# Kernel optimization log

Measured on AMD Instinct MI355X. Metric: run time of the kernel, lower is better.

## Reference

```python
import jax, jax.numpy as jnp
import numpy as np

B, S, D = 2, 2048, 2048
H = 16
I = 8192  # intermediate_size
HD = I // H  # per-head intermediate dim = 512


def setup_inputs() -> dict:
    key = jax.random.key(0)
    ks = jax.random.split(key, 7)
    scale_d = 1.0 / np.sqrt(D)
    scale_i = 1.0 / np.sqrt(I)
    return {
        "x": jax.random.normal(ks[0], (B, S, D), dtype=jnp.float32),
        "adjacency": jax.random.uniform(ks[1], (B, H, S, S), dtype=jnp.float32) * (1.0 / S),
        "Wg": jax.random.normal(ks[2], (D, I), dtype=jnp.float32) * scale_d,
        "Wu": jax.random.normal(ks[3], (D, I), dtype=jnp.float32) * scale_d,
        "Wd": jax.random.normal(ks[4], (I, D), dtype=jnp.float32) * scale_i,
        "eps": jnp.zeros((H,), dtype=jnp.float32),
        "alpha": jnp.ones((H,), dtype=jnp.float32),
    }


def reference(x, adjacency, Wg, Wu, Wd, eps, alpha):
    # gate/up projections + SwiGLU: (B,S,I)
    gate = jnp.einsum("bsd,di->bsi", x, Wg)
    up = jnp.einsum("bsd,di->bsi", x, Wu)
    h_inter = jax.nn.silu(gate) * up
    # split into heads: (B,H,S,HD)
    h_heads = h_inter.reshape(B, S, H, HD).transpose(0, 2, 1, 3)
    # batched per-head GIN: (1+eps_h)*h + alpha_h * A_h @ h, all heads at once
    agg = jnp.einsum("bhst,bhtd->bhsd", adjacency, h_heads)
    e = (1.0 + eps)[None, :, None, None]
    a = alpha[None, :, None, None]
    h_gin = e * h_heads + a * agg
    # recombine heads -> (B,S,I), then down projection
    h_comb = h_gin.transpose(0, 2, 1, 3).reshape(B, S, I)
    return jnp.einsum("bsi,id->bsd", h_comb, Wd)
```

## Files before the change

### kernel.cpp

```cpp
#include <hip/hip_runtime.h>
#include <hip/hip_bf16.h>


typedef __bf16 bf16x8 __attribute__((ext_vector_type(8)));
typedef float f32x4 __attribute__((ext_vector_type(4)));

__device__ __forceinline__ unsigned short f2bf(float f) {
    union { float f; unsigned int u; } x; x.f = f;
    unsigned int r = x.u + 0x7fffu + ((x.u >> 16) & 1u);
    return (unsigned short)(r >> 16);
}
__device__ __forceinline__ float bf2f(unsigned short b) {
    union { unsigned int u; float f; } x; x.u = ((unsigned int)b) << 16;
    return x.f;
}

__device__ __forceinline__ void gload_lds16(const void* g, void* l) {
    __builtin_amdgcn_global_load_lds((const __attribute__((address_space(1))) void*)g,
                                     (__attribute__((address_space(3))) void*)l,
                                     16, 0, 0);
}


__global__ void conv_kernel(const float* __restrict__ in, unsigned short* __restrict__ out) {
    size_t i = ((size_t)blockIdx.x * 256 + threadIdx.x) * 4;
    float4 v = *(const float4*)(in + i);
    ushort4 o; o.x = f2bf(v.x); o.y = f2bf(v.y); o.z = f2bf(v.z); o.w = f2bf(v.w);
    *(ushort4*)(out + i) = o;
}

__global__ void tconv_kernel(const float* __restrict__ in, unsigned short* __restrict__ out,
                             int R, int C) {
    __shared__ float tile[64][65];
    int nbc = C >> 6;
    int bc = blockIdx.x % nbc, br = blockIdx.x / nbc;
    int r0 = br * 64, c0 = bc * 64;
    int t = threadIdx.x;
#pragma unroll
    for (int i = 0; i < 4; ++i) {
        int idx = i * 256 + t;
        int r = idx >> 4, c4 = (idx & 15) * 4;
        float4 v = *(const float4*)(in + (size_t)(r0 + r) * C + c0 + c4);
        tile[r][c4] = v.x; tile[r][c4 + 1] = v.y; tile[r][c4 + 2] = v.z; tile[r][c4 + 3] = v.w;
    }
    __syncthreads();
#pragma unroll
    for (int i = 0; i < 4; ++i) {
        int idx = i * 256 + t;
        int c = idx >> 4, r4 = (idx & 15) * 4;
        ushort4 o;
        o.x = f2bf(tile[r4][c]); o.y = f2bf(tile[r4 + 1][c]);
        o.z = f2bf(tile[r4 + 2][c]); o.w = f2bf(tile[r4 + 3][c]);
        *(ushort4*)(out + (size_t)(c0 + c) * R + r0 + r4) = o;
    }
}

__global__ void __launch_bounds__(512, 2) gemm_gu(
    const unsigned short* __restrict__ xb,
    const unsigned short* __restrict__ WgT,
    const unsigned short* __restrict__ WuT,
    unsigned short* __restrict__ hhT)
{
    const int K = 2048;
    __shared__ unsigned short LDS[4][16384];
    int bid = (int)blockIdx.x;
    int lb = (bid & 7) * 128 + (bid >> 3);
    int mt = lb >> 6, nt = lb & 63;
    int tid = threadIdx.x, lane = tid & 63, wave = tid >> 6;
    int wm = wave >> 1, wn = wave & 1;
    int l15 = lane & 15, l4 = lane >> 4;

    f32x4 accg[4][4] = {};
    f32x4 accu[4][4] = {};

    int jl = (lane & 7) ^ (lane >> 3);
    int prowA = wave * 16 + (lane >> 3);
    int rowA0 = prowA + ((jl & 4) << 5);
    int ccA = (jl & 3) << 3;
    const unsigned short* srcA0 = xb + (size_t)(mt * 256 + rowA0) * K + ccA;
    const unsigned short* srcA1 = srcA0 + (size_t)8 * K;
    int prowB = tid >> 3;
    int jbl = (tid & 7) ^ (prowB & 7);
    int rowB0 = prowB + ((jbl & 4) << 4);
    int ccB = (jbl & 3) << 3;
    const unsigned short* srcBg = WgT + (size_t)(nt * 128 + rowB0) * K + ccB;
    const unsigned short* srcBu = WuT + (size_t)(nt * 128 + rowB0) * K + ccB;

    int cA0 = ((wm & 1) * 64 + l15) * 128 + (((((wm >> 1) << 2) + l4) ^ (l15 & 7)) << 4);
    int cB0 = l15 * 128 + ((((wn << 2) + l4) ^ (l15 & 7)) << 4);

#define GU_STAGE_A(t_) do {                                                              \
        char* dA = (char*)&LDS[(t_) & 3][0] + wave * 2048;                               \
        gload_lds16((const void*)(srcA0 + (size_t)(t_) * 32), (void*)dA);                \
        gload_lds16((const void*)(srcA1 + (size_t)(t_) * 32), (void*)(dA + 1024));       \
    } while (0)
#define GU_STAGE_B(t_) do {                                                              \
        char* dB = (char*)&LDS[(t_) & 3][8192] + wave * 1024;                            \
        gload_lds16((const void*)(srcBg + (size_t)(t_) * 32), (void*)dB);                \
        gload_lds16((const void*)(srcBu + (size_t)(t_) * 32), (void*)(dB + 8192));       \
    } while (0)

    GU_STAGE_A(0); GU_STAGE_B(0);
    GU_STAGE_A(1); GU_STAGE_B(1);
    GU_STAGE_A(2); GU_STAGE_B(2);

    for (int t = 0; t < 64; ++t) {
        if (t + 2 < 64)      asm volatile("s_waitcnt vmcnt(8)" ::: "memory");
        else if (t + 1 < 64) asm volatile("s_waitcnt vmcnt(4)" ::: "memory");
        else                 asm volatile("s_waitcnt vmcnt(0)" ::: "memory");
        __builtin_amdgcn_s_barrier();
        const char* Abase = (const char*)&LDS[t & 3][0];
        bool more = (t + 3) < 64;
        bf16x8 af[4], bfg[4], bfu[4];
#pragma unroll
        for (int ni = 0; ni < 4; ++ni) bfg[ni] = *(const bf16x8*)(Abase + 16384 + cB0 + ni * 2048);
#pragma unroll
        for (int mi = 0; mi < 4; ++mi) af[mi] = *(const bf16x8*)(Abase + cA0 + mi * 2048);
        if (more) GU_STAGE_A(t + 3);
        __builtin_amdgcn_s_barrier();
        asm volatile("s_waitcnt lgkmcnt(0)" ::: "memory");
        __builtin_amdgcn_s_setprio(1);
#pragma unroll
        for (int mi = 0; mi < 4; ++mi)
#pragma unroll
            for (int ni = 0; ni < 4; ++ni)
                accg[mi][ni] = __builtin_amdgcn_mfma_f32_16x16x32_bf16(af[mi], bfg[ni], accg[mi][ni], 0, 0, 0);
        __builtin_amdgcn_s_setprio(0);
        __builtin_amdgcn_s_barrier();
#pragma unroll
        for (int ni = 0; ni < 4; ++ni) bfu[ni] = *(const bf16x8*)(Abase + 24576 + cB0 + ni * 2048);
        if (more) GU_STAGE_B(t + 3);
        __builtin_amdgcn_s_barrier();
        asm volatile("s_waitcnt lgkmcnt(0)" ::: "memory");
        __builtin_amdgcn_s_setprio(1);
#pragma unroll
        for (int mi = 0; mi < 4; ++mi)
#pragma unroll
            for (int ni = 0; ni < 4; ++ni)
                accu[mi][ni] = __builtin_amdgcn_mfma_f32_16x16x32_bf16(af[mi], bfu[ni], accu[mi][ni], 0, 0, 0);
        __builtin_amdgcn_s_setprio(0);
    }
#undef GU_STAGE_A
#undef GU_STAGE_B

    int rowb = mt * 256 + wm * 64 + l4 * 4;
    int colb = nt * 128 + wn * 64 + l15;
    int b = mt >> 3;
#pragma unroll
    for (int mi = 0; mi < 4; ++mi)
#pragma unroll
        for (int ni = 0; ni < 4; ++ni) {
            int row = rowb + mi * 16;
            int n = colb + ni * 16;
            ushort4 hv;
#pragma unroll
            for (int r = 0; r < 4; ++r) {
                float g = accg[mi][ni][r];
                float u = accu[mi][ni][r];
                float h = g / (1.f + __expf(-g)) * u;
                ((unsigned short*)&hv)[r] = f2bf(h);
            }
            *(ushort4*)(hhT + ((size_t)b * 8192 + n) * 2048 + (row & 2047)) = hv;
        }
}

__global__ void __launch_bounds__(512, 2) gemm_agg4(
    const float* __restrict__ adj,
    const unsigned short* __restrict__ hhT,
    const float* __restrict__ eps, const float* __restrict__ alpha,
    unsigned short* __restrict__ hcomb)
{
    const int S = 2048, HD = 512, I = 8192;
    __shared__ unsigned short As[2][128 * 40];
    __shared__ unsigned short Bs[4][512 * 32];
    int bid = (int)blockIdx.x;
    int lb = (bid & 7) * 64 + (bid >> 3);
    int pair = lb >> 4;
    int mt = lb & 15;
    int b = pair >> 4, h = pair & 15;
    int tid = threadIdx.x, lane = tid & 63, wave = tid >> 6;
    int wm = wave >> 2, wn = wave & 3;
    int l15 = lane & 15, l4 = lane >> 4;
    f32x4 acc[4][8] = {};

    float e1 = 1.f + eps[h];
    float a1 = alpha[h];
    bool a1z = (a1 == 0.f);
    float dfac = a1z ? 0.f : (e1 / a1);

    const float* Ab = adj + ((size_t)pair * S + (size_t)mt * 128) * S;
    const unsigned short* Bb = hhT + ((size_t)b * I + (size_t)h * HD) * (size_t)S;

    int a_row0 = tid >> 3, a_c = (tid & 7) << 2;
    int grow0 = mt * 128 + a_row0;

    int jl = (lane & 7) ^ (lane >> 3);
    int prow0 = wave * 16 + (lane >> 3);
    int browB = prow0 + ((jl & 4) << 6);
    int ccB = (jl & 3) << 3;
    const unsigned short* srcB = Bb + (size_t)browB * S + ccB;

#define BSTAGE(t_) do {                                                           \
        char* d_ = (char*)&Bs[(t_) & 3][0] + wave * 2048;                         \
        const unsigned short* s_ = srcB + (size_t)(t_) * 32;                      \
        gload_lds16((const void*)s_, (void*)d_);                                  \
        gload_lds16((const void*)(s_ + (size_t)8 * S), (void*)(d_ + 1024));       \
        gload_lds16((const void*)(s_ + (size_t)128 * S), (void*)(d_ + 16384));    \
        gload_lds16((const void*)(s_ + (size_t)136 * S), (void*)(d_ + 17408));    \
    } while (0)

    float4 pa0_0, pa1_0, pa0_1, pa1_1;

#define ALOAD(SET, K0)                                                            \
    do {                                                                          \
        pa0_##SET = *(const float4*)(Ab + (size_t)a_row0 * S + (K0) + a_c);       \
        pa1_##SET = *(const float4*)(Ab + (size_t)(a_row0 + 64) * S + (K0) + a_c);\
    } while (0)

#define ACONV(SET, BUF, K0)                                                       \
    do {                                                                          \
        int j0 = grow0 - (K0) - a_c;                                              \
        pa0_##SET.x += (j0 == 0) ? dfac : 0.f;                                    \
        pa0_##SET.y += (j0 == 1) ? dfac : 0.f;                                    \
        pa0_##SET.z += (j0 == 2) ? dfac : 0.f;                                    \
        pa0_##SET.w += (j0 == 3) ? dfac : 0.f;                                    \
        int j1 = j0 + 64;                                                         \
        pa1_##SET.x += (j1 == 0) ? dfac : 0.f;                                    \
        pa1_##SET.y += (j1 == 1) ? dfac : 0.f;                                    \
        pa1_##SET.z += (j1 == 2) ? dfac : 0.f;                                    \
        pa1_##SET.w += (j1 == 3) ? dfac : 0.f;                                    \
        ushort4 o0, o1;                                                           \
        o0.x = f2bf(pa0_##SET.x); o0.y = f2bf(pa0_##SET.y);                       \
        o0.z = f2bf(pa0_##SET.z); o0.w = f2bf(pa0_##SET.w);                       \
        o1.x = f2bf(pa1_##SET.x); o1.y = f2bf(pa1_##SET.y);                       \
        o1.z = f2bf(pa1_##SET.z); o1.w = f2bf(pa1_##SET.w);                       \
        *(ushort4*)((char*)As[BUF] + a_row0 * 80 + a_c * 2) = o0;                 \
        *(ushort4*)((char*)As[BUF] + (a_row0 + 64) * 80 + a_c * 2) = o1;          \
    } while (0)

    int koff2 = l4 << 4;
    const char* aptr0 = (const char*)As[0] + (wm * 64 + l15) * 80 + koff2;
    const char* aptr1 = (const char*)As[1] + (wm * 64 + l15) * 80 + koff2;
    int cB = ((wn & 1) * 128 + l15) * 128 + (((l4 + ((wn >> 1) << 2)) ^ (l15 & 7)) << 4);

#define AGG_COMPUTE(APTR, BBASE)                                                        \
    do {                                                                                \
        bf16x8 af[4], bfv[8];                                                           \
        _Pragma("unroll")                                                               \
        for (int mi = 0; mi < 4; ++mi) af[mi] = *(const bf16x8*)((APTR) + mi * 16 * 80);\
        _Pragma("unroll")                                                               \
        for (int ni = 0; ni < 8; ++ni) bfv[ni] = *(const bf16x8*)((BBASE) + cB + ni * 2048);\
        __builtin_amdgcn_s_setprio(1);                                                  \
        _Pragma("unroll")                                                               \
        for (int mi = 0; mi < 4; ++mi)                                                  \
            _Pragma("unroll")                                                           \
            for (int ni = 0; ni < 8; ++ni)                                              \
                acc[mi][ni] = __builtin_amdgcn_mfma_f32_16x16x32_bf16(af[mi], bfv[ni],  \
                                                                      acc[mi][ni], 0, 0, 0); \
        __builtin_amdgcn_s_setprio(0);                                                  \
    } while (0)

    BSTAGE(0);
    ALOAD(0, 0);
    BSTAGE(1);
    ALOAD(1, 32);
    BSTAGE(2);
    ACONV(0, 0, 0);
    asm volatile("s_waitcnt lgkmcnt(0)" ::: "memory");
    __builtin_amdgcn_s_barrier();

    for (int s = 0; s < 64; s += 2) {
        AGG_COMPUTE(aptr0, (const char*)&Bs[s & 3][0]);
        ACONV(1, 1, (s + 1) * 32);
        if (s + 2 < 64) ALOAD(0, (s + 2) * 32);
        if (s + 3 < 64) BSTAGE(s + 3);
        asm volatile("s_waitcnt lgkmcnt(0)" ::: "memory");
        __builtin_amdgcn_s_barrier();
        AGG_COMPUTE(aptr1, (const char*)&Bs[(s + 1) & 3][0]);
        if (s + 2 < 64) {
            ACONV(0, 0, (s + 2) * 32);
            if (s + 3 < 64) ALOAD(1, (s + 3) * 32);
            if (s + 4 < 64) BSTAGE(s + 4);
            asm volatile("s_waitcnt lgkmcnt(0)" ::: "memory");
            __builtin_amdgcn_s_barrier();
        }
    }
#undef BSTAGE
#undef ALOAD
#undef ACONV
#undef AGG_COMPUTE

    int s_base = mt * 128 + wm * 64;
    int d_base = wn * 128;
    if (!a1z) {
#pragma unroll
        for (int mi = 0; mi < 4; ++mi)
#pragma unroll
            for (int ni = 0; ni < 8; ++ni) {
                int sb = s_base + mi * 16 + ((lane >> 4) << 2);
                int d = d_base + ni * 16 + (lane & 15);
#pragma unroll
                for (int r = 0; r < 4; ++r) {
                    size_t off = ((size_t)(b * S + sb + r)) * I + (size_t)h * HD + d;
                    hcomb[off] = f2bf(a1 * acc[mi][ni][r]);
                }
            }
    } else {
#pragma unroll
        for (int mi = 0; mi < 4; ++mi)
#pragma unroll
            for (int ni = 0; ni < 8; ++ni) {
                int sb = s_base + mi * 16 + ((lane >> 4) << 2);
                int d = d_base + ni * 16 + (lane & 15);
                size_t col = (size_t)h * HD + d;
                ushort4 hq = *(const ushort4*)(hhT + ((size_t)b * I + col) * S + sb);
#pragma unroll
                for (int r = 0; r < 4; ++r) {
                    size_t off = ((size_t)(b * S + sb + r)) * I + col;
                    hcomb[off] = f2bf(e1 * bf2f(((const unsigned short*)&hq)[r]));
                }
            }
    }
}

__global__ void __launch_bounds__(512, 2) gemm_out2(
    const unsigned short* __restrict__ hcomb,
    const unsigned short* __restrict__ WdT,
    float* __restrict__ out)
{
    const int K = 8192;
    __shared__ unsigned short LDS[6][12288];
    int bid = (int)blockIdx.x;
    int lb = (bid & 7) * 32 + (bid >> 3);
    int mt = lb >> 4, nt = lb & 15;
    int tid = threadIdx.x, lane = tid & 63, wave = tid >> 6;
    int wm = wave >> 1, wn = wave & 1;
    int l15 = lane & 15, l4 = lane >> 4;
    f32x4 acc[4][4] = {};

    int jl = (lane & 7) ^ (lane >> 3);
    int prowA = wave * 16 + (lane >> 3);
    int rowA0 = prowA + ((jl & 4) << 5);
    int ccA = (jl & 3) << 3;
    const unsigned short* srcA0 = hcomb + (size_t)(mt * 256 + rowA0) * K + ccA;
    const unsigned short* srcA1 = srcA0 + (size_t)8 * K;
    int prowB = tid >> 3;
    int jbl = (tid & 7) ^ (prowB & 7);
    int rowB0 = prowB + ((jbl & 4) << 4);
    int ccB = (jbl & 3) << 3;
    const unsigned short* srcB0 = WdT + (size_t)(nt * 128 + rowB0) * K + ccB;

    int cA0 = ((wm & 1) * 64 + l15) * 128 + (((((wm >> 1) << 2) + l4) ^ (l15 & 7)) << 4);
    int cB0 = l15 * 128 + ((((wn << 2) + l4) ^ (l15 & 7)) << 4);

#define OSTAGE(t_) do {                                                                  \
        char* dA = (char*)&LDS[(t_) % 6][0] + wave * 2048;                               \
        gload_lds16((const void*)(srcA0 + (size_t)(t_) * 32), (void*)dA);                \
        gload_lds16((const void*)(srcA1 + (size_t)(t_) * 32), (void*)(dA + 1024));       \
        char* dB = (char*)&LDS[(t_) % 6][8192] + wave * 1024;                            \
        gload_lds16((const void*)(srcB0 + (size_t)(t_) * 32), (void*)dB);                \
    } while (0)

    OSTAGE(0); OSTAGE(1); OSTAGE(2); OSTAGE(3);

    for (int t = 0; t < 256; ++t) {
        if (t + 3 < 256)      asm volatile("s_waitcnt vmcnt(9)" ::: "memory");
        else if (t + 2 < 256) asm volatile("s_waitcnt vmcnt(6)" ::: "memory");
        else if (t + 1 < 256) asm volatile("s_waitcnt vmcnt(3)" ::: "memory");
        else                  asm volatile("s_waitcnt vmcnt(0)" ::: "memory");
        __builtin_amdgcn_s_barrier();
        const char* Abase = (const char*)&LDS[t % 6][0];
        const char* Bbase = Abase + 16384;
        bool more = (t + 4) < 256;
        bf16x8 af[4], bf[4];
#pragma unroll
        for (int ni = 0; ni < 4; ++ni) bf[ni] = *(const bf16x8*)(Bbase + cB0 + ni * 2048);
        if (more) OSTAGE(t + 4);
#pragma unroll
        for (int mi = 0; mi < 4; ++mi) af[mi] = *(const bf16x8*)(Abase + cA0 + mi * 2048);
        __builtin_amdgcn_s_setprio(1);
#pragma unroll
        for (int mi = 0; mi < 4; ++mi)
#pragma unroll
            for (int ni = 0; ni < 4; ++ni)
                acc[mi][ni] = __builtin_amdgcn_mfma_f32_16x16x32_bf16(af[mi], bf[ni], acc[mi][ni], 0, 0, 0);
        __builtin_amdgcn_s_setprio(0);
    }
#undef OSTAGE

    int m_off = mt * 256 + wm * 64, n_off = nt * 128 + wn * 64;
#pragma unroll
    for (int mi = 0; mi < 4; ++mi)
#pragma unroll
        for (int ni = 0; ni < 4; ++ni) {
            int mbase = m_off + mi * 16 + l4 * 4;
            int n = n_off + ni * 16 + l15;
#pragma unroll
            for (int r = 0; r < 4; ++r)
                out[(size_t)(mbase + r) * 2048 + n] = acc[mi][ni][r];
        }
}

extern "C" void kernel_launch(void* const* d_in, const int* in_sizes, int n_in,
                              void* d_out, int out_size, void* d_ws, size_t ws_size,
                              hipStream_t stream) {
    const float* x     = (const float*)d_in[0];
    const float* adj   = (const float*)d_in[1];
    const float* Wg    = (const float*)d_in[2];
    const float* Wu    = (const float*)d_in[3];
    const float* Wd    = (const float*)d_in[4];
    const float* eps   = (const float*)d_in[5];
    const float* alpha = (const float*)d_in[6];
    float* out = (float*)d_out;

    unsigned short* ws    = (unsigned short*)d_ws;
    unsigned short* xb    = ws;
    unsigned short* WgT   = xb + (size_t)4096 * 2048;
    unsigned short* WuT   = WgT + (size_t)8192 * 2048;
    unsigned short* WdT   = WuT + (size_t)8192 * 2048;
    unsigned short* hhT   = WdT + (size_t)2048 * 8192;
    unsigned short* hcomb = hhT + (size_t)16384 * 2048;

    conv_kernel<<<8192, 256, 0, stream>>>(x, xb);
    tconv_kernel<<<4096, 256, 0, stream>>>(Wg, WgT, 2048, 8192);
    tconv_kernel<<<4096, 256, 0, stream>>>(Wu, WuT, 2048, 8192);
    tconv_kernel<<<4096, 256, 0, stream>>>(Wd, WdT, 8192, 2048);
    gemm_gu<<<1024, 512, 0, stream>>>(xb, WgT, WuT, hhT);
    gemm_agg4<<<512, 512, 0, stream>>>(adj, hhT, eps, alpha, hcomb);
    gemm_out2<<<256, 512, 0, stream>>>(hcomb, WdT, out);
}
```

Measured before the change: 692.8 us.

## Shrink LDS pipelines to double/triple buffering in gate-up and down GEMMs

The gate/up GEMM drops from a 4-stage LDS ring with split A/B staging to a 2-stage double buffer that issues the next tile at the top of each iteration. The output GEMM goes from a 6-stage ring with prefetch distance 4 to a 3-stage ring with prefetch distance 2. The smaller shared-memory footprint may allow more resident blocks and simpler waits, but it shortens prefetch distance, so global-load latency may be less well hidden.

```diff
diff --git a/kernel.cpp b/kernel.cpp
--- a/kernel.cpp
+++ b/kernel.cpp
@@ -62,7 +62,7 @@
     unsigned short* __restrict__ hhT)
 {
     const int K = 2048;
-    __shared__ unsigned short LDS[4][16384];
+    __shared__ unsigned short LDS[2][16384];
     int bid = (int)blockIdx.x;
     int lb = (bid & 7) * 128 + (bid >> 3);
     int mt = lb >> 6, nt = lb & 63;
@@ -89,50 +89,40 @@
     int cA0 = ((wm & 1) * 64 + l15) * 128 + (((((wm >> 1) << 2) + l4) ^ (l15 & 7)) << 4);
     int cB0 = l15 * 128 + ((((wn << 2) + l4) ^ (l15 & 7)) << 4);
 
-#define GU_STAGE_A(t_) do {                                                              \
-        char* dA = (char*)&LDS[(t_) & 3][0] + wave * 2048;                               \
+#define GU_STAGE(t_) do {                                                                \
+        char* dA = (char*)&LDS[(t_) & 1][0] + wave * 2048;                               \
         gload_lds16((const void*)(srcA0 + (size_t)(t_) * 32), (void*)dA);                \
         gload_lds16((const void*)(srcA1 + (size_t)(t_) * 32), (void*)(dA + 1024));       \
-    } while (0)
-#define GU_STAGE_B(t_) do {                                                              \
-        char* dB = (char*)&LDS[(t_) & 3][8192] + wave * 1024;                            \
+        char* dB = (char*)&LDS[(t_) & 1][8192] + wave * 1024;                            \
         gload_lds16((const void*)(srcBg + (size_t)(t_) * 32), (void*)dB);                \
         gload_lds16((const void*)(srcBu + (size_t)(t_) * 32), (void*)(dB + 8192));       \
     } while (0)
 
-    GU_STAGE_A(0); GU_STAGE_B(0);
-    GU_STAGE_A(1); GU_STAGE_B(1);
-    GU_STAGE_A(2); GU_STAGE_B(2);
+    GU_STAGE(0);
 
     for (int t = 0; t < 64; ++t) {
-        if (t + 2 < 64)      asm volatile("s_waitcnt vmcnt(8)" ::: "memory");
-        else if (t + 1 < 64) asm volatile("s_waitcnt vmcnt(4)" ::: "memory");
-        else                 asm volatile("s_waitcnt vmcnt(0)" ::: "memory");
         __builtin_amdgcn_s_barrier();
-        const char* Abase = (const char*)&LDS[t & 3][0];
-        bool more = (t + 3) < 64;
+        if (t + 1 < 64) {
+            GU_STAGE(t + 1);
+            asm volatile("s_waitcnt vmcnt(4)" ::: "memory");
+        } else {
+            asm volatile("s_waitcnt vmcnt(0)" ::: "memory");
+        }
+        __builtin_amdgcn_s_barrier();
+        const char* Abase = (const char*)&LDS[t & 1][0];
         bf16x8 af[4], bfg[4], bfu[4];
 #pragma unroll
+        for (int mi = 0; mi < 4; ++mi) af[mi] = *(const bf16x8*)(Abase + cA0 + mi * 2048);
+#pragma unroll
         for (int ni = 0; ni < 4; ++ni) bfg[ni] = *(const bf16x8*)(Abase + 16384 + cB0 + ni * 2048);
 #pragma unroll
-        for (int mi = 0; mi < 4; ++mi) af[mi] = *(const bf16x8*)(Abase + cA0 + mi * 2048);
-        if (more) GU_STAGE_A(t + 3);
-        __builtin_amdgcn_s_barrier();
-        asm volatile("s_waitcnt lgkmcnt(0)" ::: "memory");
+        for (int ni = 0; ni < 4; ++ni) bfu[ni] = *(const bf16x8*)(Abase + 24576 + cB0 + ni * 2048);
         __builtin_amdgcn_s_setprio(1);
 #pragma unroll
         for (int mi = 0; mi < 4; ++mi)
 #pragma unroll
             for (int ni = 0; ni < 4; ++ni)
                 accg[mi][ni] = __builtin_amdgcn_mfma_f32_16x16x32_bf16(af[mi], bfg[ni], accg[mi][ni], 0, 0, 0);
-        __builtin_amdgcn_s_setprio(0);
-        __builtin_amdgcn_s_barrier();
-#pragma unroll
-        for (int ni = 0; ni < 4; ++ni) bfu[ni] = *(const bf16x8*)(Abase + 24576 + cB0 + ni * 2048);
-        if (more) GU_STAGE_B(t + 3);
-        __builtin_amdgcn_s_barrier();
-        asm volatile("s_waitcnt lgkmcnt(0)" ::: "memory");
-        __builtin_amdgcn_s_setprio(1);
 #pragma unroll
         for (int mi = 0; mi < 4; ++mi)
 #pragma unroll
@@ -140,8 +130,7 @@
                 accu[mi][ni] = __builtin_amdgcn_mfma_f32_16x16x32_bf16(af[mi], bfu[ni], accu[mi][ni], 0, 0, 0);
         __builtin_amdgcn_s_setprio(0);
     }
-#undef GU_STAGE_A
-#undef GU_STAGE_B
+#undef GU_STAGE
 
     int rowb = mt * 256 + wm * 64 + l4 * 4;
     int colb = nt * 128 + wn * 64 + l15;
@@ -329,7 +318,7 @@
     float* __restrict__ out)
 {
     const int K = 8192;
-    __shared__ unsigned short LDS[6][12288];
+    __shared__ unsigned short LDS[3][12288];
     int bid = (int)blockIdx.x;
     int lb = (bid & 7) * 32 + (bid >> 3);
     int mt = lb >> 4, nt = lb & 15;
@@ -354,28 +343,31 @@
     int cB0 = l15 * 128 + ((((wn << 2) + l4) ^ (l15 & 7)) << 4);
 
 #define OSTAGE(t_) do {                                                                  \
-        char* dA = (char*)&LDS[(t_) % 6][0] + wave * 2048;                               \
+        char* dA = (char*)&LDS[(t_) % 3][0] + wave * 2048;                               \
         gload_lds16((const void*)(srcA0 + (size_t)(t_) * 32), (void*)dA);                \
         gload_lds16((const void*)(srcA1 + (size_t)(t_) * 32), (void*)(dA + 1024));       \
-        char* dB = (char*)&LDS[(t_) % 6][8192] + wave * 1024;                            \
+        char* dB = (char*)&LDS[(t_) % 3][8192] + wave * 1024;                            \
         gload_lds16((const void*)(srcB0 + (size_t)(t_) * 32), (void*)dB);                \
     } while (0)
 
-    OSTAGE(0); OSTAGE(1); OSTAGE(2); OSTAGE(3);
+    OSTAGE(0); OSTAGE(1);
 
     for (int t = 0; t < 256; ++t) {
-        if (t + 3 < 256)      asm volatile("s_waitcnt vmcnt(9)" ::: "memory");
-        else if (t + 2 < 256) asm volatile("s_waitcnt vmcnt(6)" ::: "memory");
-        else if (t + 1 < 256) asm volatile("s_waitcnt vmcnt(3)" ::: "memory");
-        else                  asm volatile("s_waitcnt vmcnt(0)" ::: "memory");
         __builtin_amdgcn_s_barrier();
-        const char* Abase = (const char*)&LDS[t % 6][0];
+        if (t + 2 < 256) {
+            OSTAGE(t + 2);
+            asm volatile("s_waitcnt vmcnt(6)" ::: "memory");
+        } else if (t + 1 < 256) {
+            asm volatile("s_waitcnt vmcnt(3)" ::: "memory");
+        } else {
+            asm volatile("s_waitcnt vmcnt(0)" ::: "memory");
+        }
+        __builtin_amdgcn_s_barrier();
+        const char* Abase = (const char*)&LDS[t % 3][0];
         const char* Bbase = Abase + 16384;
-        bool more = (t + 4) < 256;
         bf16x8 af[4], bf[4];
 #pragma unroll
         for (int ni = 0; ni < 4; ++ni) bf[ni] = *(const bf16x8*)(Bbase + cB0 + ni * 2048);
-        if (more) OSTAGE(t + 4);
 #pragma unroll
         for (int mi = 0; mi < 4; ++mi) af[mi] = *(const bf16x8*)(Abase + cA0 + mi * 2048);
         __builtin_amdgcn_s_setprio(1);
```

New measurement: 706.8 us. 2.0% more time.
